# Kernel optimization log

Measured on AMD Instinct MI355X. Metric: run time of the kernel, lower is better.

## Reference

```python
import jax, jax.numpy as jnp
import numpy as np

SPARSITY = 0.8
LOCAL_WINDOW = 64


def setup_inputs() -> dict:
    key = jax.random.key(0)
    k1, k2 = jax.random.split(key)
    B, H, S = 2, 8, 2048
    attention_scores = jax.random.normal(k1, (B, H, S, S), dtype=jnp.float32)
    rand_u = jax.random.uniform(k2, (B, H, S, S), dtype=jnp.float32)
    return {"attention_scores": attention_scores, "rand_u": rand_u}


def reference(attention_scores, rand_u):
    B, H, S, _ = attention_scores.shape
    dt = attention_scores.dtype
    half = LOCAL_WINDOW // 2
    k = max(1, int(S * (1.0 - SPARSITY)))

    idx = jnp.arange(S)
    # local window mask: row i covers columns [max(0,i-half), min(S,i+half))
    local = ((idx[None, :] >= idx[:, None] - half) & (idx[None, :] < idx[:, None] + half)).astype(dt)  # (S,S)

    # global mask: topk over head-averaged importance, shared across heads
    importance = attention_scores.mean(axis=1)  # (B,S,S)
    _, top_g = jax.lax.top_k(importance, k)  # (B,S,k)
    gmask = jnp.zeros((B, S, S), dtype=dt).at[
        jnp.arange(B)[:, None, None], jnp.arange(S)[None, :, None], top_g
    ].set(1.0)

    # random sparsification mask
    random_mask = (rand_u < (1.0 - SPARSITY)).astype(dt)

    combined = ((local[None, None, :, :] + gmask[:, None, :, :] + random_mask) > 0).astype(dt)

    # sparsity enforcement: per-row topk of masked scores -> binary mask
    masked = attention_scores * combined
    _, top_f = jax.lax.top_k(masked, k)  # (B,H,S,k)
    final = jnp.zeros((B, H, S, S), dtype=dt).at[
        jnp.arange(B)[:, None, None, None],
        jnp.arange(H)[None, :, None, None],
        jnp.arange(S)[None, None, :, None],
        top_f,
    ].set(1.0)
    return final
```

## Files before the change

### kernel.cpp

```cpp
#include <hip/hip_runtime.h>
#include <cstdint>
#include <cstddef>

#define S_LEN   2048
#define N_HEADS 8
#define N_BATCH 2
#define TOPK    409
#define HALF_WIN 32
#define KEY_P0  0x80000000u
#define KEY_N0  0x7FFFFFFFu
#define HIST_STRIDE 260

__device__ __forceinline__ unsigned mbcnt64(unsigned long long m) {
  return __builtin_amdgcn_mbcnt_hi((unsigned)(m >> 32),
         __builtin_amdgcn_mbcnt_lo((unsigned)m, 0u));
}

__device__ __forceinline__ unsigned mono1(float f) {
  unsigned u = __float_as_uint(f);
  return (u & 0x80000000u) ? ~u : (u | 0x80000000u);
}

__device__ __forceinline__ void radix_range(const unsigned (&keys)[32], unsigned kk0,
                                            bool pos, unsigned* h, int l,
                                            unsigned& T_ret, unsigned& kk_ret,
                                            bool& cnt1) {
  unsigned prefix = 0, done = 0, kk = kk0;
  unsigned T = 0;
  bool resolved = false;
  cnt1 = false;
  #pragma unroll
  for (int pass = 0; pass < 4; ++pass) {
    const int shift = 24 - 8 * pass;
    *(uint4*)&h[l * 4] = make_uint4(0, 0, 0, 0);
    __threadfence_block();
    #pragma unroll
    for (int q = 0; q < 32; ++q) {
      unsigned kj = keys[q];
      bool in = pos ? (kj > KEY_P0) : (kj < KEY_N0);
      if (in && (kj & done) == prefix)
        atomicAdd(&h[(kj >> shift) & 255u], 1u);
    }
    __threadfence_block();
    uint4 hv = *(const uint4*)&h[l * 4];
    unsigned s3 = hv.w;
    unsigned s2 = hv.z + s3;
    unsigned s1 = hv.y + s2;
    unsigned s0 = hv.x + s1;
    unsigned inc = s0;
    #pragma unroll
    for (int d = 1; d < 64; d <<= 1) {
      unsigned o = __shfl_down(inc, d);
      inc += (l + d < 64) ? o : 0u;
    }
    const unsigned tail = inc - s0;
    const unsigned ge[4] = {s0 + tail, s1 + tail, s2 + tail, s3 + tail};
    const unsigned gt[4] = {s1 + tail, s2 + tail, s3 + tail, tail};
    unsigned packed = 0;
    bool found = false;
    #pragma unroll
    for (int q = 0; q < 4; ++q) {
      if (gt[q] < kk && kk <= ge[q]) {
        packed = ((unsigned)(4 * l + q) << 24) | ((ge[q] - gt[q]) << 12) | (kk - gt[q]);
        found = true;
      }
    }
    unsigned long long bal = __ballot(found);
    int srcl = __ffsll((long long)bal) - 1;
    packed = __shfl(packed, srcl);
    const unsigned cnt = (packed >> 12) & 0xFFFu;
    kk = packed & 0xFFFu;
    prefix |= (packed >> 24) << shift;
    done |= 0xFFu << shift;
    if (cnt == 1u) {
      unsigned cand = 0;
      #pragma unroll
      for (int q = 0; q < 32; ++q) {
        unsigned kj = keys[q];
        bool in = pos ? (kj > KEY_P0) : (kj < KEY_N0);
        if (in && (kj & done) == prefix) cand = kj;
      }
      #pragma unroll
      for (int d = 1; d < 64; d <<= 1) cand |= __shfl_xor(cand, d);
      T = cand;
      resolved = true;
      cnt1 = true;
      break;
    }
  }
  if (!resolved) T = prefix;
  T_ret = T;
  kk_ret = kk;
}

__device__ __forceinline__ void resolve_T(const unsigned (&keys)[32], unsigned* h,
                                          int l, unsigned& T, unsigned& kk,
                                          bool& cnt1) {
  unsigned np = 0;
  #pragma unroll
  for (int q = 0; q < 32; ++q)
    np += (unsigned)__popcll(__ballot(keys[q] > KEY_P0));
  if (TOPK <= np) {
    radix_range(keys, TOPK, true, h, l, T, kk, cnt1);
  } else {
    unsigned n0 = 0, n1 = 0;
    #pragma unroll
    for (int q = 0; q < 32; ++q) {
      unsigned kj = keys[q];
      n0 += (unsigned)__popcll(__ballot(kj == KEY_P0));
      n1 += (unsigned)__popcll(__ballot(kj == KEY_N0));
    }
    if (TOPK <= np + n0)           { T = KEY_P0; kk = TOPK - np;      cnt1 = (n0 == 1); }
    else if (TOPK <= np + n0 + n1) { T = KEY_N0; kk = TOPK - np - n0; cnt1 = (n1 == 1); }
    else radix_range(keys, TOPK - np - n0 - n1, false, h, l, T, kk, cnt1);
  }
}

__device__ __forceinline__ unsigned select_bits(const unsigned (&keys)[32],
                                                unsigned T, unsigned kk,
                                                bool cnt1, int l) {
  unsigned bits = 0;
  if (cnt1) {
    #pragma unroll
    for (int q = 0; q < 32; ++q)
      bits |= (keys[q] >= T ? 1u : 0u) << q;
    return bits;
  }
  unsigned S_tot = 0;
  #pragma unroll
  for (int s = 0; s < 8; ++s) {
    unsigned long long beq[4];
    unsigned pe[4];
    #pragma unroll
    for (int e = 0; e < 4; ++e) {
      beq[e] = __ballot(keys[4 * s + e] == T);
      pe[e] = (unsigned)__popcll(beq[e]);
    }
    const unsigned th = pe[0] + pe[1] + pe[2] + pe[3];
    if (S_tot + th <= kk) {
      #pragma unroll
      for (int e = 0; e < 4; ++e)
        bits |= (keys[4 * s + e] >= T ? 1u : 0u) << (4 * s + e);
    } else if (S_tot >= kk) {
      #pragma unroll
      for (int e = 0; e < 4; ++e)
        bits |= (keys[4 * s + e] > T ? 1u : 0u) << (4 * s + e);
    } else {
      unsigned mb[4], own[4];
      #pragma unroll
      for (int e = 0; e < 4; ++e) {
        mb[e]  = mbcnt64(beq[e]);
        own[e] = (unsigned)((beq[e] >> l) & 1ull);
      }
      const unsigned cross = S_tot + mb[0] + mb[1] + mb[2] + mb[3];
      unsigned run = 0;
      #pragma unroll
      for (int e = 0; e < 4; ++e) {
        unsigned kj = keys[4 * s + e];
        bool sel = (kj > T) || (kj == T && (cross + run) < kk);
        run += own[e];
        bits |= (sel ? 1u : 0u) << (4 * s + e);
      }
    }
    S_tot += th;
  }
  return bits;
}

__global__ __launch_bounds__(512, 4) void k_fused(const float* __restrict__ scores,
                                                  const float* __restrict__ randu,
                                                  float* __restrict__ out) {
  __shared__ __align__(16) unsigned keyrow[S_LEN];
  __shared__ __align__(16) unsigned hist[8 * HIST_STRIDE];
  __shared__ unsigned gq[64];
  const int l = threadIdx.x & 63;
  const int w = threadIdx.x >> 6;
  const int bi = blockIdx.x;
  const int b = bi >> 11;
  const int i = bi & 2047;
  const size_t row = (((size_t)(b * N_HEADS + w)) * S_LEN + i) * S_LEN;
  const size_t gbase = (((size_t)(b * N_HEADS)) * S_LEN + i) * S_LEN;
  const float thr = (float)(1.0 - 0.8);
  unsigned* const h = hist + (size_t)w * HIST_STRIDE;

  unsigned sb[32];
  unsigned rndbits = 0;
  #pragma unroll
  for (int s = 0; s < 8; ++s) {
    const int j0 = 256 * s + 4 * l;
    float4 sc = *(const float4*)(scores + row + j0);
    float4 ru = *(const float4*)(randu + row + j0);
    sb[4 * s + 0] = __float_as_uint(sc.x);
    sb[4 * s + 1] = __float_as_uint(sc.y);
    sb[4 * s + 2] = __float_as_uint(sc.z);
    sb[4 * s + 3] = __float_as_uint(sc.w);
    rndbits |= (ru.x < thr ? 1u : 0u) << (4 * s + 0);
    rndbits |= (ru.y < thr ? 1u : 0u) << (4 * s + 1);
    rndbits |= (ru.z < thr ? 1u : 0u) << (4 * s + 2);
    rndbits |= (ru.w < thr ? 1u : 0u) << (4 * s + 3);
  }

  {
    const int c0 = 256 * w + 4 * l;
    float4 p = *(const float4*)(scores + gbase + c0);
    #pragma unroll
    for (int hh = 1; hh < N_HEADS; ++hh) {
      float4 x = *(const float4*)(scores + gbase + (size_t)hh * S_LEN * S_LEN + c0);
      p.x += x.x; p.y += x.y; p.z += x.z; p.w += x.w;
    }
    const float av[4] = {p.x, p.y, p.z, p.w};
    #pragma unroll
    for (int e = 0; e < 4; ++e)
      keyrow[(4 * w + e) * 64 + l] = mono1(av[e]);
  }
  __syncthreads();

  if (w == 0) {
    unsigned gk[32];
    #pragma unroll
    for (int q = 0; q < 32; ++q)
      gk[q] = keyrow[q * 64 + l];
    unsigned Tg, kkg; bool c1g;
    resolve_T(gk, hist, l, Tg, kkg, c1g);
    unsigned gbits = select_bits(gk, Tg, kkg, c1g, l);
    const int lo = i - HALF_WIN;
    #pragma unroll
    for (int q = 0; q < 32; ++q) {
      const int j = 256 * (q >> 2) + 4 * l + (q & 3);
      gbits |= ((unsigned)(j - lo) < 64u ? 1u : 0u) << q;
    }
    gq[l] = gbits;
  }
  __syncthreads();

  const unsigned combined = gq[l] | rndbits;
  #pragma unroll
  for (int q = 0; q < 32; ++q) {
    const unsigned u = sb[q];
    const unsigned m = (unsigned)((int)u >> 31) | 0x80000000u;
    const bool comb = ((combined >> q) & 1u) != 0u;
    sb[q] = (comb ? u : (u & 0x80000000u)) ^ m;
  }
  unsigned T, kk; bool c1;
  resolve_T(sb, h, l, T, kk, c1);
  unsigned bits = select_bits(sb, T, kk, c1, l);
  #pragma unroll
  for (int s = 0; s < 8; ++s) {
    float v[4] __attribute__((aligned(16)));
    #pragma unroll
    for (int e = 0; e < 4; ++e)
      v[e] = ((bits >> (4 * s + e)) & 1u) ? 1.0f : 0.0f;
    *(float4*)(out + row + 256 * s + 4 * l) = *(const float4*)v;
  }
}

extern "C" void kernel_launch(void* const* d_in, const int* in_sizes, int n_in,
                              void* d_out, int out_size, void* d_ws, size_t ws_size,
                              hipStream_t stream) {
  const float* scores = (const float*)d_in[0];
  const float* randu  = (const float*)d_in[1];
  float* out = (float*)d_out;
  (void)d_ws; (void)ws_size;
  k_fused<<<N_BATCH * S_LEN, 512, 0, stream>>>(scores, randu, out);
}
```

Baseline: 212.6 us.

## Halve block size and process two heads per wave sequentially

Blocks shrink from 512 to 256 threads (4 waves), and each wave now handles two heads in sequence instead of one. Each wave also computes two column slices of the head-summed global importance row. The second head's loads are issued after the first head's top-k selection, so they can overlap with it, and the smaller blocks with lower shared-memory use may allow more blocks per CU. The cost is more serial work per wave and a longer critical path per block.

```diff
diff --git a/kernel.cpp b/kernel.cpp
--- a/kernel.cpp
+++ b/kernel.cpp
@@ -167,41 +167,25 @@
   return bits;
 }
 
-__global__ __launch_bounds__(512, 4) void k_fused(const float* __restrict__ scores,
+__global__ __launch_bounds__(256, 6) void k_fused(const float* __restrict__ scores,
                                                   const float* __restrict__ randu,
                                                   float* __restrict__ out) {
   __shared__ __align__(16) unsigned keyrow[S_LEN];
-  __shared__ __align__(16) unsigned hist[8 * HIST_STRIDE];
+  __shared__ __align__(16) unsigned hist[4 * HIST_STRIDE];
   __shared__ unsigned gq[64];
   const int l = threadIdx.x & 63;
   const int w = threadIdx.x >> 6;
   const int bi = blockIdx.x;
   const int b = bi >> 11;
   const int i = bi & 2047;
-  const size_t row = (((size_t)(b * N_HEADS + w)) * S_LEN + i) * S_LEN;
   const size_t gbase = (((size_t)(b * N_HEADS)) * S_LEN + i) * S_LEN;
   const float thr = (float)(1.0 - 0.8);
   unsigned* const h = hist + (size_t)w * HIST_STRIDE;
 
-  unsigned sb[32];
-  unsigned rndbits = 0;
-  #pragma unroll
-  for (int s = 0; s < 8; ++s) {
-    const int j0 = 256 * s + 4 * l;
-    float4 sc = *(const float4*)(scores + row + j0);
-    float4 ru = *(const float4*)(randu + row + j0);
-    sb[4 * s + 0] = __float_as_uint(sc.x);
-    sb[4 * s + 1] = __float_as_uint(sc.y);
-    sb[4 * s + 2] = __float_as_uint(sc.z);
-    sb[4 * s + 3] = __float_as_uint(sc.w);
-    rndbits |= (ru.x < thr ? 1u : 0u) << (4 * s + 0);
-    rndbits |= (ru.y < thr ? 1u : 0u) << (4 * s + 1);
-    rndbits |= (ru.z < thr ? 1u : 0u) << (4 * s + 2);
-    rndbits |= (ru.w < thr ? 1u : 0u) << (4 * s + 3);
-  }
-
-  {
-    const int c0 = 256 * w + 4 * l;
+  #pragma unroll
+  for (int t = 0; t < 2; ++t) {
+    const int s = 2 * w + t;
+    const int c0 = 256 * s + 4 * l;
     float4 p = *(const float4*)(scores + gbase + c0);
     #pragma unroll
     for (int hh = 1; hh < N_HEADS; ++hh) {
@@ -211,7 +195,26 @@
     const float av[4] = {p.x, p.y, p.z, p.w};
     #pragma unroll
     for (int e = 0; e < 4; ++e)
-      keyrow[(4 * w + e) * 64 + l] = mono1(av[e]);
+      keyrow[(4 * s + e) * 64 + l] = mono1(av[e]);
+  }
+
+  const int hA = 2 * w;
+  const size_t rowA = gbase + (size_t)hA * S_LEN * S_LEN;
+  unsigned sbA[32];
+  unsigned rndA = 0;
+  #pragma unroll
+  for (int s = 0; s < 8; ++s) {
+    const int j0 = 256 * s + 4 * l;
+    float4 sc = *(const float4*)(scores + rowA + j0);
+    float4 ru = *(const float4*)(randu + rowA + j0);
+    sbA[4 * s + 0] = __float_as_uint(sc.x);
+    sbA[4 * s + 1] = __float_as_uint(sc.y);
+    sbA[4 * s + 2] = __float_as_uint(sc.z);
+    sbA[4 * s + 3] = __float_as_uint(sc.w);
+    rndA |= (ru.x < thr ? 1u : 0u) << (4 * s + 0);
+    rndA |= (ru.y < thr ? 1u : 0u) << (4 * s + 1);
+    rndA |= (ru.z < thr ? 1u : 0u) << (4 * s + 2);
+    rndA |= (ru.w < thr ? 1u : 0u) << (4 * s + 3);
   }
   __syncthreads();
 
@@ -232,25 +235,67 @@
     gq[l] = gbits;
   }
   __syncthreads();
-
-  const unsigned combined = gq[l] | rndbits;
-  #pragma unroll
-  for (int q = 0; q < 32; ++q) {
-    const unsigned u = sb[q];
-    const unsigned m = (unsigned)((int)u >> 31) | 0x80000000u;
-    const bool comb = ((combined >> q) & 1u) != 0u;
-    sb[q] = (comb ? u : (u & 0x80000000u)) ^ m;
-  }
-  unsigned T, kk; bool c1;
-  resolve_T(sb, h, l, T, kk, c1);
-  unsigned bits = select_bits(sb, T, kk, c1, l);
-  #pragma unroll
-  for (int s = 0; s < 8; ++s) {
-    float v[4] __attribute__((aligned(16)));
-    #pragma unroll
-    for (int e = 0; e < 4; ++e)
-      v[e] = ((bits >> (4 * s + e)) & 1u) ? 1.0f : 0.0f;
-    *(float4*)(out + row + 256 * s + 4 * l) = *(const float4*)v;
+  const unsigned gql = gq[l];
+
+  {
+    const unsigned combined = gql | rndA;
+    #pragma unroll
+    for (int q = 0; q < 32; ++q) {
+      const unsigned u = sbA[q];
+      const unsigned m = (unsigned)((int)u >> 31) | 0x80000000u;
+      const bool comb = ((combined >> q) & 1u) != 0u;
+      sbA[q] = (comb ? u : (u & 0x80000000u)) ^ m;
+    }
+    unsigned T, kk; bool c1;
+    resolve_T(sbA, h, l, T, kk, c1);
+    unsigned bits = select_bits(sbA, T, kk, c1, l);
+    #pragma unroll
+    for (int s = 0; s < 8; ++s) {
+      float v[4] __attribute__((aligned(16)));
+      #pragma unroll
+      for (int e = 0; e < 4; ++e)
+        v[e] = ((bits >> (4 * s + e)) & 1u) ? 1.0f : 0.0f;
+      *(float4*)(out + rowA + 256 * s + 4 * l) = *(const float4*)v;
+    }
+  }
+
+  {
+    const size_t rowB = rowA + (size_t)S_LEN * S_LEN;
+    unsigned sbB[32];
+    unsigned rndB = 0;
+    #pragma unroll
+    for (int s = 0; s < 8; ++s) {
+      const int j0 = 256 * s + 4 * l;
+      float4 sc = *(const float4*)(scores + rowB + j0);
+      float4 ru = *(const float4*)(randu + rowB + j0);
+      sbB[4 * s + 0] = __float_as_uint(sc.x);
+      sbB[4 * s + 1] = __float_as_uint(sc.y);
+      sbB[4 * s + 2] = __float_as_uint(sc.z);
+      sbB[4 * s + 3] = __float_as_uint(sc.w);
+      rndB |= (ru.x < thr ? 1u : 0u) << (4 * s + 0);
+      rndB |= (ru.y < thr ? 1u : 0u) << (4 * s + 1);
+      rndB |= (ru.z < thr ? 1u : 0u) << (4 * s + 2);
+      rndB |= (ru.w < thr ? 1u : 0u) << (4 * s + 3);
+    }
+    const unsigned combined = gql | rndB;
+    #pragma unroll
+    for (int q = 0; q < 32; ++q) {
+      const unsigned u = sbB[q];
+      const unsigned m = (unsigned)((int)u >> 31) | 0x80000000u;
+      const bool comb = ((combined >> q) & 1u) != 0u;
+      sbB[q] = (comb ? u : (u & 0x80000000u)) ^ m;
+    }
+    unsigned T, kk; bool c1;
+    resolve_T(sbB, h, l, T, kk, c1);
+    unsigned bits = select_bits(sbB, T, kk, c1, l);
+    #pragma unroll
+    for (int s = 0; s < 8; ++s) {
+      float v[4] __attribute__((aligned(16)));
+      #pragma unroll
+      for (int e = 0; e < 4; ++e)
+        v[e] = ((bits >> (4 * s + e)) & 1u) ? 1.0f : 0.0f;
+      *(float4*)(out + rowB + 256 * s + 4 * l) = *(const float4*)v;
+    }
   }
 }
 
@@ -261,5 +306,5 @@
   const float* randu  = (const float*)d_in[1];
   float* out = (float*)d_out;
   (void)d_ws; (void)ws_size;
-  k_fused<<<N_BATCH * S_LEN, 512, 0, stream>>>(scores, randu, out);
-}
+  k_fused<<<N_BATCH * S_LEN, 256, 0, stream>>>(scores, randu, out);
+}
```

Result: slower. 273.8 us (+28.8%).

## Halve block size so each wave processes two heads sequentially

Applied to the files above, without the earlier changes.

The block shrinks from 512 to 256 threads, and each of the four waves now handles two heads one after another instead of one head per wave. The head-averaging step also covers two column slices per wave. The per-head scores load moves after the global top-k, which removes the early prefetch that overlapped with the head-mean and global selection. The aim is to raise occupancy by using fewer registers and less LDS per block, at the cost of serialised per-wave work and lost overlap of loads.

```diff
diff --git a/kernel.cpp b/kernel.cpp
--- a/kernel.cpp
+++ b/kernel.cpp
@@ -167,41 +167,25 @@
   return bits;
 }
 
-__global__ __launch_bounds__(512, 4) void k_fused(const float* __restrict__ scores,
+__global__ __launch_bounds__(256, 4) void k_fused(const float* __restrict__ scores,
                                                   const float* __restrict__ randu,
                                                   float* __restrict__ out) {
   __shared__ __align__(16) unsigned keyrow[S_LEN];
-  __shared__ __align__(16) unsigned hist[8 * HIST_STRIDE];
+  __shared__ __align__(16) unsigned hist[4 * HIST_STRIDE];
   __shared__ unsigned gq[64];
   const int l = threadIdx.x & 63;
   const int w = threadIdx.x >> 6;
   const int bi = blockIdx.x;
   const int b = bi >> 11;
   const int i = bi & 2047;
-  const size_t row = (((size_t)(b * N_HEADS + w)) * S_LEN + i) * S_LEN;
   const size_t gbase = (((size_t)(b * N_HEADS)) * S_LEN + i) * S_LEN;
   const float thr = (float)(1.0 - 0.8);
   unsigned* const h = hist + (size_t)w * HIST_STRIDE;
 
-  unsigned sb[32];
-  unsigned rndbits = 0;
-  #pragma unroll
-  for (int s = 0; s < 8; ++s) {
-    const int j0 = 256 * s + 4 * l;
-    float4 sc = *(const float4*)(scores + row + j0);
-    float4 ru = *(const float4*)(randu + row + j0);
-    sb[4 * s + 0] = __float_as_uint(sc.x);
-    sb[4 * s + 1] = __float_as_uint(sc.y);
-    sb[4 * s + 2] = __float_as_uint(sc.z);
-    sb[4 * s + 3] = __float_as_uint(sc.w);
-    rndbits |= (ru.x < thr ? 1u : 0u) << (4 * s + 0);
-    rndbits |= (ru.y < thr ? 1u : 0u) << (4 * s + 1);
-    rndbits |= (ru.z < thr ? 1u : 0u) << (4 * s + 2);
-    rndbits |= (ru.w < thr ? 1u : 0u) << (4 * s + 3);
-  }
-
-  {
-    const int c0 = 256 * w + 4 * l;
+  #pragma unroll
+  for (int t = 0; t < 2; ++t) {
+    const int s = 2 * w + t;
+    const int c0 = 256 * s + 4 * l;
     float4 p = *(const float4*)(scores + gbase + c0);
     #pragma unroll
     for (int hh = 1; hh < N_HEADS; ++hh) {
@@ -211,7 +195,7 @@
     const float av[4] = {p.x, p.y, p.z, p.w};
     #pragma unroll
     for (int e = 0; e < 4; ++e)
-      keyrow[(4 * w + e) * 64 + l] = mono1(av[e]);
+      keyrow[(4 * s + e) * 64 + l] = mono1(av[e]);
   }
   __syncthreads();
 
@@ -232,25 +216,47 @@
     gq[l] = gbits;
   }
   __syncthreads();
-
-  const unsigned combined = gq[l] | rndbits;
-  #pragma unroll
-  for (int q = 0; q < 32; ++q) {
-    const unsigned u = sb[q];
-    const unsigned m = (unsigned)((int)u >> 31) | 0x80000000u;
-    const bool comb = ((combined >> q) & 1u) != 0u;
-    sb[q] = (comb ? u : (u & 0x80000000u)) ^ m;
-  }
-  unsigned T, kk; bool c1;
-  resolve_T(sb, h, l, T, kk, c1);
-  unsigned bits = select_bits(sb, T, kk, c1, l);
-  #pragma unroll
-  for (int s = 0; s < 8; ++s) {
-    float v[4] __attribute__((aligned(16)));
-    #pragma unroll
-    for (int e = 0; e < 4; ++e)
-      v[e] = ((bits >> (4 * s + e)) & 1u) ? 1.0f : 0.0f;
-    *(float4*)(out + row + 256 * s + 4 * l) = *(const float4*)v;
+  const unsigned gql = gq[l];
+
+  #pragma unroll 1
+  for (int t = 0; t < 2; ++t) {
+    const int hh = 2 * w + t;
+    const size_t rowh = gbase + (size_t)hh * S_LEN * S_LEN;
+    unsigned sb[32];
+    unsigned rnd = 0;
+    #pragma unroll
+    for (int s = 0; s < 8; ++s) {
+      const int j0 = 256 * s + 4 * l;
+      float4 sc = *(const float4*)(scores + rowh + j0);
+      float4 ru = *(const float4*)(randu + rowh + j0);
+      sb[4 * s + 0] = __float_as_uint(sc.x);
+      sb[4 * s + 1] = __float_as_uint(sc.y);
+      sb[4 * s + 2] = __float_as_uint(sc.z);
+      sb[4 * s + 3] = __float_as_uint(sc.w);
+      rnd |= (ru.x < thr ? 1u : 0u) << (4 * s + 0);
+      rnd |= (ru.y < thr ? 1u : 0u) << (4 * s + 1);
+      rnd |= (ru.z < thr ? 1u : 0u) << (4 * s + 2);
+      rnd |= (ru.w < thr ? 1u : 0u) << (4 * s + 3);
+    }
+    const unsigned combined = gql | rnd;
+    #pragma unroll
+    for (int q = 0; q < 32; ++q) {
+      const unsigned u = sb[q];
+      const unsigned m = (unsigned)((int)u >> 31) | 0x80000000u;
+      const bool comb = ((combined >> q) & 1u) != 0u;
+      sb[q] = (comb ? u : (u & 0x80000000u)) ^ m;
+    }
+    unsigned T, kk; bool c1;
+    resolve_T(sb, h, l, T, kk, c1);
+    unsigned bits = select_bits(sb, T, kk, c1, l);
+    #pragma unroll
+    for (int s = 0; s < 8; ++s) {
+      float v[4] __attribute__((aligned(16)));
+      #pragma unroll
+      for (int e = 0; e < 4; ++e)
+        v[e] = ((bits >> (4 * s + e)) & 1u) ? 1.0f : 0.0f;
+      *(float4*)(out + rowh + 256 * s + 4 * l) = *(const float4*)v;
+    }
   }
 }
 
@@ -261,5 +267,5 @@
   const float* randu  = (const float*)d_in[1];
   float* out = (float*)d_out;
   (void)d_ws; (void)ws_size;
-  k_fused<<<N_BATCH * S_LEN, 512, 0, stream>>>(scores, randu, out);
-}
+  k_fused<<<N_BATCH * S_LEN, 256, 0, stream>>>(scores, randu, out);
+}
```

Measured after the change: 200.2 us. 5.9% less time.
